# Kernel tuning notes

Measured on AMD Instinct MI355X. Metric: run time of the kernel, lower is better.

Reference implementation:

```python
import jax, jax.numpy as jnp
from jax import lax
import numpy as np

NEG_SLOPE = 0.01  # PyTorch LeakyReLU default


def setup_inputs() -> dict:
    key = jax.random.key(0)
    ks = jax.random.split(key, 7)
    B, Ns, T, C = 32, 512, 128, 25
    proj_dim, H = 20, 25
    s_lin = 1.0 / np.sqrt(C)
    s_gru = 1.0 / np.sqrt(H)
    return {
        "x": jax.random.normal(ks[0], (B, Ns, T, C), jnp.float32),
        "W1": jax.random.uniform(ks[1], (proj_dim, C), jnp.float32, -s_lin, s_lin),
        "b1": jax.random.uniform(ks[2], (proj_dim,), jnp.float32, -s_lin, s_lin),
        "W_ih": jax.random.uniform(ks[3], (3 * H, proj_dim), jnp.float32, -s_gru, s_gru),
        "W_hh": jax.random.uniform(ks[4], (3 * H, H), jnp.float32, -s_gru, s_gru),
        "b_ih": jax.random.uniform(ks[5], (3 * H,), jnp.float32, -s_gru, s_gru),
        "b_hh": jax.random.uniform(ks[6], (3 * H,), jnp.float32, -s_gru, s_gru),
    }


def reference(x, W1, b1, W_ih, W_hh, b_ih, b_hh):
    # Linear + LeakyReLU projection: [B, Ns, T, 25] -> [B, Ns, T, proj_dim]
    p = jnp.einsum("bntc,pc->bntp", x, W1) + b1
    p = jnp.where(p >= 0, p, NEG_SLOPE * p)

    B, Ns, T, P = p.shape
    H = W_hh.shape[1]
    p = p.reshape(B * Ns, T, P)

    # Precompute input-side gate pre-activations for all timesteps: [N, T, 3H]
    gx = jnp.einsum("ntp,gp->ntg", p, W_ih) + b_ih
    gx = jnp.swapaxes(gx, 0, 1)  # [T, N, 3H] for scan

    def step(h, gx_t):
        gh = h @ W_hh.T + b_hh  # [N, 3H]
        xr, xz, xn = jnp.split(gx_t, 3, axis=-1)
        hr, hz, hn = jnp.split(gh, 3, axis=-1)
        r = jax.nn.sigmoid(xr + hr)
        z = jax.nn.sigmoid(xz + hz)
        n = jnp.tanh(xn + r * hn)
        h_new = (1.0 - z) * n + z * h
        return h_new, None

    h0 = jnp.zeros((B * Ns, H), p.dtype)
    hT, _ = lax.scan(step, h0, gx)
    return hT.reshape(B, Ns, H)
```

## Files before the change

### kernel.cpp

```cpp
#include <hip/hip_runtime.h>


typedef __bf16 bf16x8 __attribute__((ext_vector_type(8)));
typedef float  f32x4  __attribute__((ext_vector_type(4)));

#define TT 128
#define CC 25
#define PP 20
#define HH 25
#define NSEQ 16384
#define S  36

__device__ __forceinline__ void split2(float f, __bf16& hi, __bf16& lo) {
    hi = (__bf16)f;
    lo = (__bf16)(f - (float)hi);
}
__device__ __forceinline__ float sigm(float v) { return 1.f / (1.f + __expf(-v)); }

__global__ __launch_bounds__(64, 1) void gru_mfma_t(
    const float* __restrict__ x,   const float* __restrict__ W1,
    const float* __restrict__ b1,  const float* __restrict__ Wih,
    const float* __restrict__ Whh, const float* __restrict__ bih,
    const float* __restrict__ bhh, float* __restrict__ out)
{
    __shared__ float sp[16 * S];
    __shared__ float sh[2][16 * S];

    const int lane = threadIdx.x;
    const int m = lane & 15, q = lane >> 4;
    const int n0 = blockIdx.x * 16;

    for (int idx = lane; idx < 16 * S; idx += 64) {
        sp[idx] = 0.f; sh[0][idx] = 0.f; sh[1][idx] = 0.f;
    }
    __syncthreads();
    if (lane < 16) {
        sp[lane * S + PP]    = 1.0f;
        sh[0][lane * S + HH] = 1.0f;
        sh[1][lane * S + HH] = 1.0f;
    }
    __syncthreads();

    bf16x8 WihH[6], WihL[6], WhhH[6], WhhL[6], W1H[2], W1L[2];
    #pragma unroll
    for (int tt = 0; tt < 6; ++tt) {
        const int g = tt >> 1;
        const int u = (tt & 1) * 16 + m;
        const bool uv = (u < HH);
        const int row = g * HH + u;
        bf16x8 ih, il, hh, hl;
        #pragma unroll
        for (int j = 0; j < 8; ++j) {
            const int k = q * 8 + j;
            float vih = 0.f, vhh = 0.f;
            if (uv) {
                if (k < PP)       vih = Wih[row * PP + k];
                else if (k == PP) vih = bih[row];
                if (k < HH)       vhh = Whh[row * HH + k];
                else if (k == HH) vhh = bhh[row];
            }
            __bf16 a, b;
            split2(vih, a, b); ih[j] = a; il[j] = b;
            split2(vhh, a, b); hh[j] = a; hl[j] = b;
        }
        WihH[tt] = ih; WihL[tt] = il; WhhH[tt] = hh; WhhL[tt] = hl;
    }
    #pragma unroll
    for (int tt = 0; tt < 2; ++tt) {
        const int u = tt * 16 + m;
        const bool uv = (u < PP);
        bf16x8 h8, l8;
        #pragma unroll
        for (int j = 0; j < 8; ++j) {
            const int k = q * 8 + j;
            float v = 0.f;
            if (uv) {
                if (k < CC)       v = W1[u * CC + k];
                else if (k == CC) v = b1[u];
            }
            __bf16 a, b; split2(v, a, b); h8[j] = a; l8[j] = b;
        }
        W1H[tt] = h8; W1L[tt] = l8;
    }

    const float* xrow = x + (size_t)(n0 + m) * (TT * CC);
    float xc[8];
    #pragma unroll
    for (int j = 0; j < 8; ++j) {
        const int k = q * 8 + j;
        xc[j] = (k < CC) ? xrow[k] : (k == CC ? 1.0f : 0.f);
    }

    float ho[2][4] = {{0.f,0.f,0.f,0.f},{0.f,0.f,0.f,0.f}};

    for (int t = 0; t < TT; ++t) {
        bf16x8 xH, xL;
        #pragma unroll
        for (int j = 0; j < 8; ++j) { __bf16 a,b; split2(xc[j],a,b); xH[j]=a; xL[j]=b; }

        if (t + 1 < TT) {
            const float* xr = xrow + (t + 1) * CC;
            #pragma unroll
            for (int j = 0; j < 8; ++j) {
                const int k = q * 8 + j;
                if (k < CC) xc[j] = xr[k];
            }
        }

        f32x4 p0 = {0.f,0.f,0.f,0.f}, p1 = {0.f,0.f,0.f,0.f};
        p0 = __builtin_amdgcn_mfma_f32_16x16x32_bf16(W1H[0], xH, p0, 0,0,0);
        p0 = __builtin_amdgcn_mfma_f32_16x16x32_bf16(W1H[0], xL, p0, 0,0,0);
        p0 = __builtin_amdgcn_mfma_f32_16x16x32_bf16(W1L[0], xH, p0, 0,0,0);
        p1 = __builtin_amdgcn_mfma_f32_16x16x32_bf16(W1H[1], xH, p1, 0,0,0);
        p1 = __builtin_amdgcn_mfma_f32_16x16x32_bf16(W1H[1], xL, p1, 0,0,0);
        p1 = __builtin_amdgcn_mfma_f32_16x16x32_bf16(W1L[1], xH, p1, 0,0,0);

        #pragma unroll
        for (int r = 0; r < 4; ++r) {
            p0[r] = (p0[r] >= 0.f) ? p0[r] : 0.01f * p0[r];
            p1[r] = (p1[r] >= 0.f) ? p1[r] : 0.01f * p1[r];
        }

        *(f32x4*)(sp + m * S + 4 * q) = p0;
        if (q == 0) *(f32x4*)(sp + m * S + 16) = p1;

        f32x4 pa = ((const f32x4*)(sp + m * S + 8 * q))[0];
        f32x4 pb = ((const f32x4*)(sp + m * S + 8 * q))[1];
        bf16x8 pH, pL;
        #pragma unroll
        for (int j = 0; j < 4; ++j) {
            __bf16 a,b;
            split2(pa[j], a, b); pH[j]   = a; pL[j]   = b;
            split2(pb[j], a, b); pH[4+j] = a; pL[4+j] = b;
        }
        f32x4 ha = ((const f32x4*)(sh[t & 1] + m * S + 8 * q))[0];
        f32x4 hb = ((const f32x4*)(sh[t & 1] + m * S + 8 * q))[1];
        bf16x8 hH, hL;
        #pragma unroll
        for (int j = 0; j < 4; ++j) {
            __bf16 a,b;
            split2(ha[j], a, b); hH[j]   = a; hL[j]   = b;
            split2(hb[j], a, b); hH[4+j] = a; hL[4+j] = b;
        }

        f32x4 aR[2], aZ[2], aN[2], aHn[2];
        #pragma unroll
        for (int tp = 0; tp < 2; ++tp) {
            f32x4 acc = {0.f,0.f,0.f,0.f};
            acc = __builtin_amdgcn_mfma_f32_16x16x32_bf16(WihH[tp], pH, acc, 0,0,0);
            acc = __builtin_amdgcn_mfma_f32_16x16x32_bf16(WihH[tp], pL, acc, 0,0,0);
            acc = __builtin_amdgcn_mfma_f32_16x16x32_bf16(WihL[tp], pH, acc, 0,0,0);
            acc = __builtin_amdgcn_mfma_f32_16x16x32_bf16(WhhH[tp], hH, acc, 0,0,0);
            acc = __builtin_amdgcn_mfma_f32_16x16x32_bf16(WhhH[tp], hL, acc, 0,0,0);
            acc = __builtin_amdgcn_mfma_f32_16x16x32_bf16(WhhL[tp], hH, acc, 0,0,0);
            aR[tp] = acc;
            f32x4 az = {0.f,0.f,0.f,0.f};
            az = __builtin_amdgcn_mfma_f32_16x16x32_bf16(WihH[2+tp], pH, az, 0,0,0);
            az = __builtin_amdgcn_mfma_f32_16x16x32_bf16(WihH[2+tp], pL, az, 0,0,0);
            az = __builtin_amdgcn_mfma_f32_16x16x32_bf16(WihL[2+tp], pH, az, 0,0,0);
            az = __builtin_amdgcn_mfma_f32_16x16x32_bf16(WhhH[2+tp], hH, az, 0,0,0);
            az = __builtin_amdgcn_mfma_f32_16x16x32_bf16(WhhH[2+tp], hL, az, 0,0,0);
            az = __builtin_amdgcn_mfma_f32_16x16x32_bf16(WhhL[2+tp], hH, az, 0,0,0);
            aZ[tp] = az;
            f32x4 an = {0.f,0.f,0.f,0.f};
            an = __builtin_amdgcn_mfma_f32_16x16x32_bf16(WihH[4+tp], pH, an, 0,0,0);
            an = __builtin_amdgcn_mfma_f32_16x16x32_bf16(WihH[4+tp], pL, an, 0,0,0);
            an = __builtin_amdgcn_mfma_f32_16x16x32_bf16(WihL[4+tp], pH, an, 0,0,0);
            aN[tp] = an;
            f32x4 ah = {0.f,0.f,0.f,0.f};
            ah = __builtin_amdgcn_mfma_f32_16x16x32_bf16(WhhH[4+tp], hH, ah, 0,0,0);
            ah = __builtin_amdgcn_mfma_f32_16x16x32_bf16(WhhH[4+tp], hL, ah, 0,0,0);
            ah = __builtin_amdgcn_mfma_f32_16x16x32_bf16(WhhL[4+tp], hH, ah, 0,0,0);
            aHn[tp] = ah;
        }

        #pragma unroll
        for (int tp = 0; tp < 2; ++tp) {
            f32x4 hv;
            #pragma unroll
            for (int r = 0; r < 4; ++r) {
                const float rg = sigm(aR[tp][r]);
                const float zg = sigm(aZ[tp][r]);
                const float nv = aN[tp][r] + rg * aHn[tp][r];
                const float e  = __expf(-2.f * nv);
                const float ng = 2.f / (1.f + e) - 1.f;
                const float h2 = zg * (ho[tp][r] - ng) + ng;
                ho[tp][r] = h2; hv[r] = h2;
            }
            float* dst = sh[(t + 1) & 1] + m * S + tp * 16 + 4 * q;
            if (tp == 0) {
                *(f32x4*)dst = hv;
            } else {
                if (q < 2)       *(f32x4*)dst = hv;
                else if (q == 2) dst[0] = hv[0];
            }
        }
    }

    float* orow = out + (size_t)(n0 + m) * HH;
    #pragma unroll
    for (int tp = 0; tp < 2; ++tp) {
        #pragma unroll
        for (int r = 0; r < 4; ++r) {
            const int u = tp * 16 + 4 * q + r;
            if (u < HH) orow[u] = ho[tp][r];
        }
    }
}

extern "C" void kernel_launch(void* const* d_in, const int* in_sizes, int n_in,
                              void* d_out, int out_size, void* d_ws, size_t ws_size,
                              hipStream_t stream) {
    const float* x   = (const float*)d_in[0];
    const float* W1  = (const float*)d_in[1];
    const float* b1  = (const float*)d_in[2];
    const float* Wih = (const float*)d_in[3];
    const float* Whh = (const float*)d_in[4];
    const float* bih = (const float*)d_in[5];
    const float* bhh = (const float*)d_in[6];
    float* out = (float*)d_out;

    gru_mfma_t<<<NSEQ / 16, 64, 0, stream>>>(x, W1, b1, Wih, Whh, bih, bhh, out);
}
```

Before: 430.9 us.

## Software-pipeline input-gate MFMAs one timestep ahead of the recurrent step

Splits each timestep into an input-side part (x projection, LeakyReLU, W_ih gate pre-activations) and a recurrent part (W_hh MFMAs and gate math). The input-side work for step t+1 is issued before the recurrent step t, using two ping-pong GX register buffers, with the loop unrolled by two. The aim is to let independent MFMA work fill the latency of the serial hidden-state dependency chain, since each CU runs only a few single-wave blocks. In exchange it raises register pressure and does one redundant gate computation at the tail.

```diff
diff --git a/kernel.cpp b/kernel.cpp
--- a/kernel.cpp
+++ b/kernel.cpp
@@ -10,6 +10,7 @@
 #define HH 25
 #define NSEQ 16384
 #define S  36
+#define MFMA __builtin_amdgcn_mfma_f32_16x16x32_bf16
 
 __device__ __forceinline__ void split2(float f, __bf16& hi, __bf16& lo) {
     hi = (__bf16)f;
@@ -91,15 +92,15 @@
         xc[j] = (k < CC) ? xrow[k] : (k == CC ? 1.0f : 0.f);
     }
 
-    float ho[2][4] = {{0.f,0.f,0.f,0.f},{0.f,0.f,0.f,0.f}};
-
-    for (int t = 0; t < TT; ++t) {
+    struct GX { f32x4 r[2], z[2], n[2]; };
+
+    auto compute_gx = [&](int tn, GX& g) {
         bf16x8 xH, xL;
         #pragma unroll
         for (int j = 0; j < 8; ++j) { __bf16 a,b; split2(xc[j],a,b); xH[j]=a; xL[j]=b; }
 
-        if (t + 1 < TT) {
-            const float* xr = xrow + (t + 1) * CC;
+        {
+            const float* xr = xrow + tn * CC;
             #pragma unroll
             for (int j = 0; j < 8; ++j) {
                 const int k = q * 8 + j;
@@ -108,13 +109,12 @@
         }
 
         f32x4 p0 = {0.f,0.f,0.f,0.f}, p1 = {0.f,0.f,0.f,0.f};
-        p0 = __builtin_amdgcn_mfma_f32_16x16x32_bf16(W1H[0], xH, p0, 0,0,0);
-        p0 = __builtin_amdgcn_mfma_f32_16x16x32_bf16(W1H[0], xL, p0, 0,0,0);
-        p0 = __builtin_amdgcn_mfma_f32_16x16x32_bf16(W1L[0], xH, p0, 0,0,0);
-        p1 = __builtin_amdgcn_mfma_f32_16x16x32_bf16(W1H[1], xH, p1, 0,0,0);
-        p1 = __builtin_amdgcn_mfma_f32_16x16x32_bf16(W1H[1], xL, p1, 0,0,0);
-        p1 = __builtin_amdgcn_mfma_f32_16x16x32_bf16(W1L[1], xH, p1, 0,0,0);
-
+        p0 = MFMA(W1H[0], xH, p0, 0,0,0);
+        p0 = MFMA(W1H[0], xL, p0, 0,0,0);
+        p0 = MFMA(W1L[0], xH, p0, 0,0,0);
+        p1 = MFMA(W1H[1], xH, p1, 0,0,0);
+        p1 = MFMA(W1H[1], xL, p1, 0,0,0);
+        p1 = MFMA(W1L[1], xH, p1, 0,0,0);
         #pragma unroll
         for (int r = 0; r < 4; ++r) {
             p0[r] = (p0[r] >= 0.f) ? p0[r] : 0.01f * p0[r];
@@ -129,51 +129,63 @@
         bf16x8 pH, pL;
         #pragma unroll
         for (int j = 0; j < 4; ++j) {
-            __bf16 a,b;
+            __bf16 a, b;
             split2(pa[j], a, b); pH[j]   = a; pL[j]   = b;
             split2(pb[j], a, b); pH[4+j] = a; pL[4+j] = b;
         }
-        f32x4 ha = ((const f32x4*)(sh[t & 1] + m * S + 8 * q))[0];
-        f32x4 hb = ((const f32x4*)(sh[t & 1] + m * S + 8 * q))[1];
+
+        #pragma unroll
+        for (int tp = 0; tp < 2; ++tp) {
+            f32x4 acc = {0.f,0.f,0.f,0.f};
+            acc = MFMA(WihH[tp], pH, acc, 0,0,0);
+            acc = MFMA(WihH[tp], pL, acc, 0,0,0);
+            acc = MFMA(WihL[tp], pH, acc, 0,0,0);
+            g.r[tp] = acc;
+            f32x4 az = {0.f,0.f,0.f,0.f};
+            az = MFMA(WihH[2+tp], pH, az, 0,0,0);
+            az = MFMA(WihH[2+tp], pL, az, 0,0,0);
+            az = MFMA(WihL[2+tp], pH, az, 0,0,0);
+            g.z[tp] = az;
+            f32x4 an = {0.f,0.f,0.f,0.f};
+            an = MFMA(WihH[4+tp], pH, an, 0,0,0);
+            an = MFMA(WihH[4+tp], pL, an, 0,0,0);
+            an = MFMA(WihL[4+tp], pH, an, 0,0,0);
+            g.n[tp] = an;
+        }
+    };
+
+    float ho[2][4] = {{0.f,0.f,0.f,0.f},{0.f,0.f,0.f,0.f}};
+
+    auto gru_step = [&](int t, const GX& g) {
+        const float* hrow = sh[t & 1] + m * S + 8 * q;
+        f32x4 ha = ((const f32x4*)hrow)[0];
+        f32x4 hb = ((const f32x4*)hrow)[1];
         bf16x8 hH, hL;
         #pragma unroll
         for (int j = 0; j < 4; ++j) {
-            __bf16 a,b;
+            __bf16 a, b;
             split2(ha[j], a, b); hH[j]   = a; hL[j]   = b;
             split2(hb[j], a, b); hH[4+j] = a; hL[4+j] = b;
         }
-
-        f32x4 aR[2], aZ[2], aN[2], aHn[2];
+        f32x4 aR[2], aZ[2], aHn[2];
         #pragma unroll
         for (int tp = 0; tp < 2; ++tp) {
-            f32x4 acc = {0.f,0.f,0.f,0.f};
-            acc = __builtin_amdgcn_mfma_f32_16x16x32_bf16(WihH[tp], pH, acc, 0,0,0);
-            acc = __builtin_amdgcn_mfma_f32_16x16x32_bf16(WihH[tp], pL, acc, 0,0,0);
-            acc = __builtin_amdgcn_mfma_f32_16x16x32_bf16(WihL[tp], pH, acc, 0,0,0);
-            acc = __builtin_amdgcn_mfma_f32_16x16x32_bf16(WhhH[tp], hH, acc, 0,0,0);
-            acc = __builtin_amdgcn_mfma_f32_16x16x32_bf16(WhhH[tp], hL, acc, 0,0,0);
-            acc = __builtin_amdgcn_mfma_f32_16x16x32_bf16(WhhL[tp], hH, acc, 0,0,0);
+            f32x4 acc = g.r[tp];
+            acc = MFMA(WhhH[tp], hH, acc, 0,0,0);
+            acc = MFMA(WhhH[tp], hL, acc, 0,0,0);
+            acc = MFMA(WhhL[tp], hH, acc, 0,0,0);
             aR[tp] = acc;
-            f32x4 az = {0.f,0.f,0.f,0.f};
-            az = __builtin_amdgcn_mfma_f32_16x16x32_bf16(WihH[2+tp], pH, az, 0,0,0);
-            az = __builtin_amdgcn_mfma_f32_16x16x32_bf16(WihH[2+tp], pL, az, 0,0,0);
-            az = __builtin_amdgcn_mfma_f32_16x16x32_bf16(WihL[2+tp], pH, az, 0,0,0);
-            az = __builtin_amdgcn_mfma_f32_16x16x32_bf16(WhhH[2+tp], hH, az, 0,0,0);
-            az = __builtin_amdgcn_mfma_f32_16x16x32_bf16(WhhH[2+tp], hL, az, 0,0,0);
-            az = __builtin_amdgcn_mfma_f32_16x16x32_bf16(WhhL[2+tp], hH, az, 0,0,0);
+            f32x4 az = g.z[tp];
+            az = MFMA(WhhH[2+tp], hH, az, 0,0,0);
+            az = MFMA(WhhH[2+tp], hL, az, 0,0,0);
+            az = MFMA(WhhL[2+tp], hH, az, 0,0,0);
             aZ[tp] = az;
-            f32x4 an = {0.f,0.f,0.f,0.f};
-            an = __builtin_amdgcn_mfma_f32_16x16x32_bf16(WihH[4+tp], pH, an, 0,0,0);
-            an = __builtin_amdgcn_mfma_f32_16x16x32_bf16(WihH[4+tp], pL, an, 0,0,0);
-            an = __builtin_amdgcn_mfma_f32_16x16x32_bf16(WihL[4+tp], pH, an, 0,0,0);
-            aN[tp] = an;
             f32x4 ah = {0.f,0.f,0.f,0.f};
-            ah = __builtin_amdgcn_mfma_f32_16x16x32_bf16(WhhH[4+tp], hH, ah, 0,0,0);
-            ah = __builtin_amdgcn_mfma_f32_16x16x32_bf16(WhhH[4+tp], hL, ah, 0,0,0);
-            ah = __builtin_amdgcn_mfma_f32_16x16x32_bf16(WhhL[4+tp], hH, ah, 0,0,0);
+            ah = MFMA(WhhH[4+tp], hH, ah, 0,0,0);
+            ah = MFMA(WhhH[4+tp], hL, ah, 0,0,0);
+            ah = MFMA(WhhL[4+tp], hH, ah, 0,0,0);
             aHn[tp] = ah;
         }
-
         #pragma unroll
         for (int tp = 0; tp < 2; ++tp) {
             f32x4 hv;
@@ -181,7 +193,7 @@
             for (int r = 0; r < 4; ++r) {
                 const float rg = sigm(aR[tp][r]);
                 const float zg = sigm(aZ[tp][r]);
-                const float nv = aN[tp][r] + rg * aHn[tp][r];
+                const float nv = g.n[tp][r] + rg * aHn[tp][r];
                 const float e  = __expf(-2.f * nv);
                 const float ng = 2.f / (1.f + e) - 1.f;
                 const float h2 = zg * (ho[tp][r] - ng) + ng;
@@ -195,6 +207,18 @@
                 else if (q == 2) dst[0] = hv[0];
             }
         }
+    };
+
+    GX A, B;
+    compute_gx(1, A);
+
+    for (int t = 0; t < TT; t += 2) {
+        const int t2 = (t + 2 < TT) ? t + 2 : TT - 1;
+        const int t3 = (t + 3 < TT) ? t + 3 : TT - 1;
+        compute_gx(t2, B);
+        gru_step(t, A);
+        compute_gx(t3, A);
+        gru_step(t + 1, B);
     }
 
     float* orow = out + (size_t)(n0 + m) * HH;
```

Result: faster. 421.7 us (-2.1%).
